# Kernel optimization log

Hardware: AMD Instinct MI355X
Metric: run time of the kernel (lower is better)

Reference implementation:

```python
import jax, jax.numpy as jnp
import numpy as np

B, NP, L, C, NA = 16, 512, 20, 3, 50
RATIO = 0.8
K = int(np.ceil(RATIO * NP))  # 410 nodes kept per graph
N = B * NP
E = 6 * N
NF, EF = 13, 4
EPS = 1e-5


def _graph_norm(x, w, b, ms):
    # PyG GraphNorm called WITHOUT batch in the source -> single global graph
    mean = x.mean(0)
    out = x - ms * mean
    var = (out * out).mean(0)
    return w * out / jnp.sqrt(var + EPS) + b


def _forward(x, pan_w, lin1_w, lin1_b, norm1_w, norm1_b, norm1_ms,
             pool_p, pool_beta, gat_wl, gat_bl, gat_wr, gat_br, gat_att, gat_bias,
             norm2_w, norm2_b, norm2_ms,
             val1_w, val1_b, val2_w, val2_b, val3_w, val3_b,
             adv1_w, adv1_b, adv2_w, adv2_b, adv3_w, adv3_b,
             edge_index, current_node_ids, action_mask):
    src, dst = edge_index[0], edge_index[1]
    # PANConv builds SparseTensor(row=edge_index[1], col=edge_index[0]) -> row = target
    A = jnp.zeros((B, NP, NP), x.dtype).at[dst // NP, dst % NP, src % NP].set(1.0)
    eyeB = jnp.broadcast_to(jnp.eye(NP, dtype=x.dtype), A.shape)

    # panentropy: M = sum_{i=0..L} w_i * A^i  (dense per graph)
    def step(carry, wi):
        tmp, acc = carry
        tmp = tmp @ A
        return (tmp, acc + wi * tmp), None
    (_, M), _ = jax.lax.scan(step, (eyeB, pan_w[0] * eyeB), pan_w[1:])
    deg = M.sum(-1)                                   # row sums
    dis = jnp.where(deg > 0, 1.0 / jnp.sqrt(deg), 0.0)
    Mn = dis[:, :, None] * M * dis[:, None, :]        # D^-1/2 M D^-1/2

    # conv1: propagate (Mn @ x) then Linear
    x3 = x.reshape(B, NP, NF)
    h = jnp.einsum('bij,bjf->bif', Mn, x3) @ lin1_w + lin1_b   # [B,NP,C]
    x1 = jax.nn.relu(_graph_norm(h.reshape(N, C), norm1_w, norm1_b, norm1_ms))  # [N,C]
    h = x1.reshape(B, NP, C)

    # PANPooling: score = tanh(b0 * <x,p> + b1 * colsum(Mn)); keep top K per graph
    score = jnp.tanh(pool_beta[0] * (h * pool_p).sum(-1) + pool_beta[1] * Mn.sum(-2))
    vals, idx = jax.lax.top_k(score, K)                        # [B,K]
    xp = jnp.take_along_axis(h, idx[:, :, None], axis=1) * vals[..., None]
    Mg = jax.vmap(lambda m, i: m[i][:, i])(Mn, idx)            # filtered adjacency [B,K,K]
    mask = (jnp.swapaxes(Mg, 1, 2) != 0) | jnp.eye(K, dtype=bool)  # mask[b,i,j]: edge j->i (+self loops)

    # GATv2Conv, heads=1, eval mode (no dropout), edge_attr not passed in source
    xl = xp @ gat_wl + gat_bl
    xr = xp @ gat_wr + gat_br
    e = jax.nn.leaky_relu(xr[:, :, None, :] + xl[:, None, :, :], 0.2)  # [B,i,j,C]
    logits = jnp.where(mask, jnp.einsum('bijc,c->bij', e, gat_att), -1e9)
    alpha = jax.nn.softmax(logits, axis=-1)
    g = jnp.einsum('bij,bjc->bic', alpha, xl) + gat_bias

    g = jax.nn.relu(_graph_norm(g.reshape(B * K, C), norm2_w, norm2_b, norm2_ms)).reshape(B, K, C)
    gp = g.sum(1)                                              # global_add_pool [B,C]

    # source uses POOLED bincount cumsum offsets to index the pre-pool arrays (faithful)
    gidx = current_node_ids + jnp.arange(B, dtype=current_node_ids.dtype) * K
    feat = jnp.concatenate([x[gidx], x1[gidx], gp], axis=1)    # [B,19]

    a = jax.nn.relu(feat @ adv1_w + adv1_b)
    a = jax.nn.relu(a @ adv2_w + adv2_b)
    a = a @ adv3_w + adv3_b
    v = jax.nn.relu(feat @ val1_w + val1_b)
    v = jax.nn.relu(v @ val2_w + val2_b)
    v = v @ val3_w + val3_b
    q = v + (a - a.mean(1, keepdims=True))
    return jnp.where(action_mask == 0, -1e8, q)


def setup_inputs() -> dict:
    key = jax.random.key(0)
    ks = list(jax.random.split(key, 40))
    nk = lambda: ks.pop()
    # within-graph random edges so the PyG-style batch structure is valid
    g = jax.random.randint(nk(), (E,), 0, B)
    u = jax.random.randint(nk(), (E,), 0, NP)
    v = jax.random.randint(nk(), (E,), 0, NP)
    edge_index = jnp.stack([g * NP + u, g * NP + v]).astype(jnp.int32)

    def lin(k, i, o):
        k1, k2 = jax.random.split(k)
        return (jax.random.normal(k1, (i, o), jnp.float32) / np.sqrt(i),
                jax.random.normal(k2, (o,), jnp.float32) * 0.01)

    lin1_w, lin1_b = lin(nk(), NF, C)
    gat_wl, gat_bl = lin(nk(), C, C)
    gat_wr, gat_br = lin(nk(), C, C)
    val1_w, val1_b = lin(nk(), 19, 10)
    val2_w, val2_b = lin(nk(), 10, 5)
    val3_w, val3_b = lin(nk(), 5, 1)
    adv1_w, adv1_b = lin(nk(), 19, 10)
    adv2_w, adv2_b = lin(nk(), 10, 5)
    adv3_w, adv3_b = lin(nk(), 5, NA)
    return dict(
        x=jax.random.normal(nk(), (N, NF), jnp.float32),
        edge_index=edge_index,
        edge_attr=jax.random.normal(nk(), (E, EF), jnp.float32),
        batch=jnp.arange(N, dtype=jnp.int32) // NP,
        current_node_ids=jax.random.randint(nk(), (B,), 0, NP),
        action_mask=jax.random.randint(nk(), (B, NA), 0, 2),
        pan_w=jax.random.uniform(nk(), (L + 1,), jnp.float32) * 0.5,
        lin1_w=lin1_w, lin1_b=lin1_b,
        norm1_w=jnp.ones(C), norm1_b=jnp.zeros(C), norm1_ms=jnp.ones(C),
        pool_p=jax.random.normal(nk(), (C,), jnp.float32),
        pool_beta=jnp.array([0.5, 0.5], jnp.float32),
        gat_wl=gat_wl, gat_bl=gat_bl, gat_wr=gat_wr, gat_br=gat_br,
        gat_att=jax.random.normal(nk(), (C,), jnp.float32),
        gat_bias=jax.random.normal(nk(), (C,), jnp.float32) * 0.01,
        norm2_w=jnp.ones(C), norm2_b=jnp.zeros(C), norm2_ms=jnp.ones(C),
        val1_w=val1_w, val1_b=val1_b, val2_w=val2_w, val2_b=val2_b,
        val3_w=val3_w, val3_b=val3_b,
        adv1_w=adv1_w, adv1_b=adv1_b, adv2_w=adv2_w, adv2_b=adv2_b,
        adv3_w=adv3_w, adv3_b=adv3_b,
    )


def reference(x, edge_index, edge_attr, batch, current_node_ids, action_mask,
              pan_w, lin1_w, lin1_b, norm1_w, norm1_b, norm1_ms,
              pool_p, pool_beta, gat_wl, gat_bl, gat_wr, gat_br, gat_att, gat_bias,
              norm2_w, norm2_b, norm2_ms,
              val1_w, val1_b, val2_w, val2_b, val3_w, val3_b,
              adv1_w, adv1_b, adv2_w, adv2_b, adv3_w, adv3_b):
    del edge_attr, batch  # received by the torch forward but never consumed
    return _forward(x, pan_w, lin1_w, lin1_b, norm1_w, norm1_b, norm1_ms,
                    pool_p, pool_beta, gat_wl, gat_bl, gat_wr, gat_br, gat_att, gat_bias,
                    norm2_w, norm2_b, norm2_ms,
                    val1_w, val1_b, val2_w, val2_b, val3_w, val3_b,
                    adv1_w, adv1_b, adv2_w, adv2_b, adv3_w, adv3_b,
                    edge_index, current_node_ids, action_mask)
```

## Files before the change

kernel.cpp:

```cpp
#include <hip/hip_runtime.h>
#include <hip/hip_bf16.h>
#include <stdint.h>
#include <math.h>

#define BB   16
#define NPn  512
#define LLp  20
#define NAa  50
#define KKk  410
#define NNt  (BB * NPn)
#define EEe  (6 * NNt)
#define NFf  13
#define KPAD 416
#define EPSf 1e-5f
#define QCLMP 1e6f
#define MAXD 28
#define PADR 512

__device__ __forceinline__ float r12_sane(float v) {
    if (!(v == v)) return 0.0f;
    return fminf(fmaxf(v, -1e15f), 1e15f);
}

__global__ __launch_bounds__(256) void r12_scatter(
    const int* __restrict__ ei,
    uint32_t* __restrict__ fwdb, uint32_t* __restrict__ trsb)
{
    const int e = blockIdx.x * 256 + threadIdx.x;
    if (e < EEe) {
        const int src = ei[e], dst = ei[EEe + e];
        atomicOr(&fwdb[(size_t)dst * 16 + ((src & 511) >> 5)], 1u << (src & 31));
        atomicOr(&trsb[(size_t)src * 16 + ((dst & 511) >> 5)], 1u << (dst & 31));
    }
}

__global__ __launch_bounds__(256) void r12_extract(
    const uint32_t* __restrict__ fwdb, const uint32_t* __restrict__ trsb,
    unsigned short* __restrict__ csrF, unsigned short* __restrict__ csrT)
{
    const int t = blockIdx.x * 256 + threadIdx.x;
    const int node = t & 8191;
    const uint32_t* bs = (t < 8192) ? (fwdb + (size_t)node * 16)
                                    : (trsb + (size_t)node * 16);
    unsigned short* cs = (t < 8192) ? csrF : csrT;
    int cnt = 0;
    for (int w = 0; w < 16; ++w) {
        uint32_t bits = bs[w];
        while (bits) {
            const int u = (w << 5) + __ffs(bits) - 1;
            bits &= bits - 1;
            if (cnt < MAXD) cs[(size_t)cnt * 8192 + node] = (unsigned short)u;
            ++cnt;
        }
    }
    for (int j = cnt; j < MAXD; ++j) cs[(size_t)j * 8192 + node] = PADR;
}

__global__ __launch_bounds__(512) void r12_deg(
    const unsigned short* __restrict__ csrF,
    const float* __restrict__ panw,
    float* __restrict__ disv)
{
    __shared__ float pa[513], pb[513];
    __shared__ float wsh[21];
    const int b = blockIdx.x, v = threadIdx.x;
    const int node = b * 512 + v;
    int iF[MAXD];
#pragma unroll
    for (int j = 0; j < MAXD; ++j) iF[j] = (int)csrF[(size_t)j * 8192 + node];
    if (v < 21) wsh[v] = panw[v];
    pa[v] = 1.0f;
    if (v == 0) { pa[512] = 0.0f; pb[512] = 0.0f; }
    __syncthreads();
    float dacc = wsh[0];
    float* rp = pa; float* rn = pb;
    for (int i = 1; i <= LLp; ++i) {
        float t[MAXD];
#pragma unroll
        for (int j = 0; j < MAXD; ++j) t[j] = rp[iF[j]];
        float s = 0.0f;
#pragma unroll
        for (int j = 0; j < MAXD; ++j) s += t[j];
        rn[v] = s;
        dacc += wsh[i] * s;
        __syncthreads();
        float* tp = rp; rp = rn; rn = tp;
    }
    disv[node] = (dacc > 0.0f) ? 1.0f / sqrtf(dacc) : 0.0f;
}

__global__ __launch_bounds__(512) void r12_chan(
    const float* __restrict__ x,
    const unsigned short* __restrict__ csrF,
    const unsigned short* __restrict__ csrT,
    const float* __restrict__ disv,
    const float* __restrict__ panw,
    const float* __restrict__ l1w,
    const float* __restrict__ l1b,
    float* __restrict__ h_raw,
    float* __restrict__ colsum)
{
    __shared__ float pa[513], pb[513];
    __shared__ float wsh[21];
    const int b = blockIdx.x, c = blockIdx.y, v = threadIdx.x;
    const int node = b * 512 + v;
    const unsigned short* csr = (c < 3) ? csrF : csrT;
    int idx[MAXD];
#pragma unroll
    for (int j = 0; j < MAXD; ++j) idx[j] = (int)csr[(size_t)j * 8192 + node];
    if (v < 21) wsh[v] = panw[v];
    const float d0 = disv[node];

    float seed;
    if (c < 3) {
        float xw = 0.0f;
        const float* xr = x + (size_t)node * NFf;
        for (int f = 0; f < NFf; ++f) xw += xr[f] * l1w[f * 3 + c];
        seed = d0 * xw;
    } else {
        seed = d0;
    }
    pa[v] = seed;
    if (v == 0) { pa[512] = 0.0f; pb[512] = 0.0f; }
    __syncthreads();
    float acc = wsh[0] * seed;
    float* rp = pa; float* rn = pb;
    for (int i = 1; i <= LLp; ++i) {
        float t[MAXD];
#pragma unroll
        for (int j = 0; j < MAXD; ++j) t[j] = rp[idx[j]];
        float s = 0.0f;
#pragma unroll
        for (int j = 0; j < MAXD; ++j) s += t[j];
        rn[v] = s;
        acc += wsh[i] * s;
        __syncthreads();
        float* tp = rp; rp = rn; rn = tp;
    }
    if (c < 3) h_raw[(size_t)node * 3 + c] = r12_sane(d0 * acc + l1b[c]);
    else       colsum[node] = r12_sane(d0 * acc);
}

__global__ __launch_bounds__(512) void r12_closure(
    const unsigned short* __restrict__ csrF, uint32_t* __restrict__ Rb)
{
    __shared__ uint32_t R1[513], R2[513];
    const int b = blockIdx.x, q = blockIdx.y, v = threadIdx.x;
    const int node = b * 512 + v;
    int iF[MAXD];
#pragma unroll
    for (int j = 0; j < MAXD; ++j) iF[j] = (int)csrF[(size_t)j * 8192 + node];
    R1[v] = ((v >> 5) == q) ? (1u << (v & 31)) : 0u;
    if (v == 0) { R1[512] = 0u; R2[512] = 0u; }
    __syncthreads();
    uint32_t* Rp = R1; uint32_t* Rn = R2;
    for (int i = 0; i < LLp; ++i) {
        uint32_t t[MAXD];
#pragma unroll
        for (int j = 0; j < MAXD; ++j) t[j] = Rp[iF[j]];
        uint32_t r = Rp[v];
#pragma unroll
        for (int j = 0; j < MAXD; ++j) r |= t[j];
        Rn[v] = r;
        __syncthreads();
        uint32_t* tp = Rp; Rp = Rn; Rn = tp;
    }
    Rb[(size_t)node * 16 + q] = Rp[v];
}

__global__ __launch_bounds__(512) void r12_pool(
    const float* __restrict__ h_raw,
    const float* __restrict__ colsum,
    const float* n1w, const float* n1b, const float* n1ms,
    const float* poolp, const float* poolb,
    float* __restrict__ x1,
    float* __restrict__ xp,
    int* __restrict__ kept)
{
    __shared__ float red[512];
    __shared__ float mv[6];
    __shared__ float sc[NPn];
    const int b = blockIdx.x, v = threadIdx.x;
    const float inv_n = 1.0f / (float)NNt;

    float hv0[16], hv1[16], hv2[16];
    float s0 = 0.0f, s1 = 0.0f, s2 = 0.0f;
#pragma unroll
    for (int k = 0; k < 16; ++k) {
        const float* hr = h_raw + (size_t)(k * 512 + v) * 3;
        hv0[k] = hr[0]; hv1[k] = hr[1]; hv2[k] = hr[2];
        s0 += hv0[k]; s1 += hv1[k]; s2 += hv2[k];
    }
    float acc[3] = { s0, s1, s2 };
    for (int c = 0; c < 3; ++c) {
        __syncthreads();
        red[v] = acc[c];
        __syncthreads();
        for (int st = 256; st > 0; st >>= 1) {
            if (v < st) red[v] += red[v + st];
            __syncthreads();
        }
        if (v == 0) mv[c] = red[0] * inv_n;
    }
    __syncthreads();
    const float mm0 = n1ms[0] * mv[0], mm1 = n1ms[1] * mv[1], mm2 = n1ms[2] * mv[2];
    float a0 = 0.0f, a1 = 0.0f, a2 = 0.0f;
#pragma unroll
    for (int k = 0; k < 16; ++k) {
        const float d0 = hv0[k] - mm0, d1 = hv1[k] - mm1, d2 = hv2[k] - mm2;
        a0 += d0 * d0; a1 += d1 * d1; a2 += d2 * d2;
    }
    float accv[3] = { a0, a1, a2 };
    for (int c = 0; c < 3; ++c) {
        __syncthreads();
        red[v] = accv[c];
        __syncthreads();
        for (int st = 256; st > 0; st >>= 1) {
            if (v < st) red[v] += red[v + st];
            __syncthreads();
        }
        if (v == 0) mv[3 + c] = red[0] * inv_n;
    }
    __syncthreads();

    const float mmv[3] = { mm0, mm1, mm2 };
    float xv[3];
#pragma unroll
    for (int c = 0; c < 3; ++c) {
        const float iv = 1.0f / sqrtf(fmaxf(mv[3 + c], 0.0f) + EPSf);
        const float o  = h_raw[(size_t)(b * NPn + v) * 3 + c] - mmv[c];
        const float tt = n1w[c] * o * iv + n1b[c];
        xv[c] = fmaxf(tt, 0.0f);
        x1[(size_t)(b * NPn + v) * 3 + c] = xv[c];
    }
    float s = poolb[0] * (xv[0] * poolp[0] + xv[1] * poolp[1] + xv[2] * poolp[2])
            + poolb[1] * colsum[b * NPn + v];
    s = tanhf(s);
    if (!(s == s)) s = 0.0f;
    sc[v] = s;
    __syncthreads();
    int cnt = 0;
    for (int u = 0; u < NPn; ++u) {
        const float su = sc[u];
        cnt += ((su > s) || (su == s && u < v)) ? 1 : 0;
    }
    if (cnt < KKk) {
        kept[b * KPAD + cnt] = v;
        xp[(size_t)(b * KPAD + cnt) * 3 + 0] = xv[0] * s;
        xp[(size_t)(b * KPAD + cnt) * 3 + 1] = xv[1] * s;
        xp[(size_t)(b * KPAD + cnt) * 3 + 2] = xv[2] * s;
    }
}

__global__ __launch_bounds__(512) void r12_gat(
    const float* __restrict__ xp,
    const int* __restrict__ kept,
    const uint32_t* __restrict__ Rb,
    const float* wl, const float* bl,
    const float* wr, const float* br,
    const float* att, const float* gbias,
    float* __restrict__ g_raw)
{
    __shared__ float xlS[KKk * 3];
    __shared__ int kidx[KPAD];
    __shared__ uint32_t RT[16 * KPAD];
    const int b = blockIdx.x, t = threadIdx.x;
    const int lane = t & 63, wv = t >> 6;
    const int wid = blockIdx.y * 8 + wv;

    float Wl[9], Wr[9];
#pragma unroll
    for (int i2 = 0; i2 < 9; ++i2) { Wl[i2] = wl[i2]; Wr[i2] = wr[i2]; }
    const float Bl0 = bl[0], Bl1 = bl[1], Bl2 = bl[2];
    const float Br0 = br[0], Br1 = br[1], Br2 = br[2];
    const float At0 = att[0], At1 = att[1], At2 = att[2];
    const float Gb0 = gbias[0], Gb1 = gbias[1], Gb2 = gbias[2];

    for (int j = t; j < KKk; j += 512) {
        const int vj = kept[b * KPAD + j];
        kidx[j] = vj;
        const float p0 = xp[(size_t)(b * KPAD + j) * 3 + 0];
        const float p1 = xp[(size_t)(b * KPAD + j) * 3 + 1];
        const float p2 = xp[(size_t)(b * KPAD + j) * 3 + 2];
        xlS[j * 3 + 0] = p0 * Wl[0] + p1 * Wl[3] + p2 * Wl[6] + Bl0;
        xlS[j * 3 + 1] = p0 * Wl[1] + p1 * Wl[4] + p2 * Wl[7] + Bl1;
        xlS[j * 3 + 2] = p0 * Wl[2] + p1 * Wl[5] + p2 * Wl[8] + Bl2;
        const uint32_t* rr = Rb + (size_t)(b * NPn + vj) * 16;
#pragma unroll
        for (int w = 0; w < 16; ++w) RT[w * KPAD + j] = rr[w];
    }
    __syncthreads();

    for (int i = wid; i < KKk; i += 32) {
        const float p0 = xp[(size_t)(b * KPAD + i) * 3 + 0];
        const float p1 = xp[(size_t)(b * KPAD + i) * 3 + 1];
        const float p2 = xp[(size_t)(b * KPAD + i) * 3 + 2];
        const float xr0 = p0 * Wr[0] + p1 * Wr[3] + p2 * Wr[6] + Br0;
        const float xr1 = p0 * Wr[1] + p1 * Wr[4] + p2 * Wr[7] + Br1;
        const float xr2 = p0 * Wr[2] + p1 * Wr[5] + p2 * Wr[8] + Br2;
        const int bi = kidx[i];
        const uint32_t mbit = 1u << (bi & 31);
        const uint32_t* Rw = &RT[(bi >> 5) * KPAD];

        float mx = -3e38f, lsum = 0.0f, a0 = 0.0f, a1 = 0.0f, a2 = 0.0f;
        for (int j = lane; j < KKk; j += 64) {
            if ((Rw[j] & mbit) || (j == i)) {
                float e0 = xr0 + xlS[j * 3 + 0]; e0 = e0 > 0.0f ? e0 : 0.2f * e0;
                float e1 = xr1 + xlS[j * 3 + 1]; e1 = e1 > 0.0f ? e1 : 0.2f * e1;
                float e2 = xr2 + xlS[j * 3 + 2]; e2 = e2 > 0.0f ? e2 : 0.2f * e2;
                const float s = At0 * e0 + At1 * e1 + At2 * e2;
                if (s > mx) {
                    const float r = __expf(mx - s);
                    lsum *= r; a0 *= r; a1 *= r; a2 *= r;
                    mx = s;
                }
                const float pj = __expf(s - mx);
                lsum += pj;
                a0 += pj * xlS[j * 3 + 0];
                a1 += pj * xlS[j * 3 + 1];
                a2 += pj * xlS[j * 3 + 2];
            }
        }
        for (int off = 32; off; off >>= 1) {
            const float mo = __shfl_xor(mx, off);
            const float lo = __shfl_xor(lsum, off);
            const float b0 = __shfl_xor(a0, off);
            const float b1 = __shfl_xor(a1, off);
            const float b2 = __shfl_xor(a2, off);
            const float M  = fmaxf(mx, mo);
            const float ea = __expf(mx - M), eb = __expf(mo - M);
            lsum = lsum * ea + lo * eb;
            a0 = a0 * ea + b0 * eb;
            a1 = a1 * ea + b1 * eb;
            a2 = a2 * ea + b2 * eb;
            mx = M;
        }
        if (lane == 0) {
            const float rl = 1.0f / fmaxf(lsum, 1e-30f);
            g_raw[(size_t)(b * KPAD + i) * 3 + 0] = r12_sane(a0 * rl + Gb0);
            g_raw[(size_t)(b * KPAD + i) * 3 + 1] = r12_sane(a1 * rl + Gb1);
            g_raw[(size_t)(b * KPAD + i) * 3 + 2] = r12_sane(a2 * rl + Gb2);
        }
    }
}

__global__ __launch_bounds__(512) void r12_head(
    const float* __restrict__ g_raw,
    const float* __restrict__ x1,
    const float* __restrict__ x,
    const int* __restrict__ cnid,
    const int* __restrict__ amask,
    const float* n2w, const float* n2b, const float* n2ms,
    const float* v1w, const float* v1b,
    const float* v2w, const float* v2b,
    const float* v3w, const float* v3b,
    const float* a1w, const float* a1b,
    const float* a2w, const float* a2b,
    const float* a3w, const float* a3b,
    float* __restrict__ out)
{
    __shared__ float rbuf[512];
    __shared__ float mv[6];
    __shared__ float gp[3];
    __shared__ float feat[19];
    __shared__ float h1a[10], h1v[10], h2a[5], h2v[5];
    __shared__ float a3[50];
    __shared__ float vout_s, amean_s;
    const int b = blockIdx.x, t = threadIdx.x;
    const float denom = 1.0f / (float)(BB * KKk);

    float gv0[13], gv1[13], gv2[13];
    float s0 = 0.0f, s1 = 0.0f, s2 = 0.0f;
#pragma unroll
    for (int k = 0; k < 13; ++k) {
        const int r = k * 512 + t;
        float q0 = 0.0f, q1 = 0.0f, q2 = 0.0f;
        if (r < BB * KKk) {
            const int bq = r / KKk, iq = r - bq * KKk;
            const float* gr = g_raw + (size_t)(bq * KPAD + iq) * 3;
            q0 = gr[0]; q1 = gr[1]; q2 = gr[2];
        }
        gv0[k] = q0; gv1[k] = q1; gv2[k] = q2;
        s0 += q0; s1 += q1; s2 += q2;
    }
    float acc[3] = { s0, s1, s2 };
    for (int c = 0; c < 3; ++c) {
        __syncthreads();
        rbuf[t] = acc[c];
        __syncthreads();
        for (int st = 256; st > 0; st >>= 1) {
            if (t < st) rbuf[t] += rbuf[t + st];
            __syncthreads();
        }
        if (t == 0) mv[c] = rbuf[0] * denom;
    }
    __syncthreads();
    const float mm0 = n2ms[0] * mv[0], mm1 = n2ms[1] * mv[1], mm2 = n2ms[2] * mv[2];
    float a0 = 0.0f, a1 = 0.0f, a2 = 0.0f;
#pragma unroll
    for (int k = 0; k < 13; ++k) {
        const int r = k * 512 + t;
        if (r < BB * KKk) {
            const float d0 = gv0[k] - mm0, d1 = gv1[k] - mm1, d2 = gv2[k] - mm2;
            a0 += d0 * d0; a1 += d1 * d1; a2 += d2 * d2;
        }
    }
    float accv[3] = { a0, a1, a2 };
    for (int c = 0; c < 3; ++c) {
        __syncthreads();
        rbuf[t] = accv[c];
        __syncthreads();
        for (int st = 256; st > 0; st >>= 1) {
            if (t < st) rbuf[t] += rbuf[t + st];
            __syncthreads();
        }
        if (t == 0) mv[3 + c] = rbuf[0] * denom;
    }
    __syncthreads();

    const float mmv[3] = { mm0, mm1, mm2 };
    float s3[3] = { 0.0f, 0.0f, 0.0f };
    if (t < KKk) {
        const size_t r = (size_t)(b * KPAD + t) * 3;
#pragma unroll
        for (int c = 0; c < 3; ++c) {
            const float iv = 1.0f / sqrtf(fmaxf(mv[3 + c], 0.0f) + EPSf);
            s3[c] = fmaxf((g_raw[r + c] - mmv[c]) * iv * n2w[c] + n2b[c], 0.0f);
        }
    }
    for (int c = 0; c < 3; ++c) {
        __syncthreads();
        rbuf[t] = s3[c];
        __syncthreads();
        for (int st = 256; st > 0; st >>= 1) {
            if (t < st) rbuf[t] += rbuf[t + st];
            __syncthreads();
        }
        if (t == 0) gp[c] = rbuf[0];
    }
    __syncthreads();

    if (t < 19) {
        const int gidx = cnid[b] + b * KKk;
        float fv;
        if (t < 13)      fv = x[(size_t)gidx * NFf + t];
        else if (t < 16) fv = x1[(size_t)gidx * 3 + (t - 13)];
        else             fv = gp[t - 16];
        feat[t] = fv;
    }
    __syncthreads();

    if (t < 10) {
        float s = a1b[t];
        for (int f = 0; f < 19; ++f) s += feat[f] * a1w[f * 10 + t];
        h1a[t] = fmaxf(s, 0.0f);
    } else if (t >= 64 && t < 74) {
        const int j = t - 64;
        float s = v1b[j];
        for (int f = 0; f < 19; ++f) s += feat[f] * v1w[f * 10 + j];
        h1v[j] = fmaxf(s, 0.0f);
    }
    __syncthreads();
    if (t < 5) {
        float s = a2b[t];
        for (int k = 0; k < 10; ++k) s += h1a[k] * a2w[k * 5 + t];
        h2a[t] = fmaxf(s, 0.0f);
    } else if (t >= 64 && t < 69) {
        const int j = t - 64;
        float s = v2b[j];
        for (int k = 0; k < 10; ++k) s += h1v[k] * v2w[k * 5 + j];
        h2v[j] = fmaxf(s, 0.0f);
    }
    __syncthreads();
    if (t < 50) {
        float s = a3b[t];
        for (int k = 0; k < 5; ++k) s += h2a[k] * a3w[k * 50 + t];
        a3[t] = s;
    } else if (t == 64) {
        float s = v3b[0];
        for (int k = 0; k < 5; ++k) s += h2v[k] * v3w[k];
        vout_s = s;
    }
    __syncthreads();
    if (t == 0) {
        float s = 0.0f;
        for (int k = 0; k < 50; ++k) s += a3[k];
        amean_s = s * (1.0f / 50.0f);
    }
    __syncthreads();
    if (t < 50) {
        float q = vout_s + a3[t] - amean_s;
        if (!(q == q)) q = 0.0f;
        q = fminf(fmaxf(q, -QCLMP), QCLMP);
        out[b * NAa + t] = (amask[b * NAa + t] == 0) ? -1e8f : q;
    }
}

extern "C" void kernel_launch(void* const* d_in, const int* in_sizes, int n_in,
                              void* d_out, int out_size, void* d_ws, size_t ws_size,
                              hipStream_t stream) {
    (void)in_sizes; (void)n_in; (void)out_size;
    const float* x     = (const float*)d_in[0];
    const int* ei      = (const int*)d_in[1];
    const int* cnid    = (const int*)d_in[4];
    const int* amask   = (const int*)d_in[5];
    const float* panw  = (const float*)d_in[6];
    const float* l1w   = (const float*)d_in[7];
    const float* l1b   = (const float*)d_in[8];
    const float* n1w   = (const float*)d_in[9];
    const float* n1b   = (const float*)d_in[10];
    const float* n1ms  = (const float*)d_in[11];
    const float* poolp = (const float*)d_in[12];
    const float* poolb = (const float*)d_in[13];
    const float* gwl   = (const float*)d_in[14];
    const float* gbl   = (const float*)d_in[15];
    const float* gwr   = (const float*)d_in[16];
    const float* gbr   = (const float*)d_in[17];
    const float* gatt  = (const float*)d_in[18];
    const float* gbias = (const float*)d_in[19];
    const float* n2w   = (const float*)d_in[20];
    const float* n2b   = (const float*)d_in[21];
    const float* n2ms  = (const float*)d_in[22];
    const float* v1w   = (const float*)d_in[23];
    const float* v1b   = (const float*)d_in[24];
    const float* v2w   = (const float*)d_in[25];
    const float* v2b   = (const float*)d_in[26];
    const float* v3w   = (const float*)d_in[27];
    const float* v3b   = (const float*)d_in[28];
    const float* a1w   = (const float*)d_in[29];
    const float* a1b   = (const float*)d_in[30];
    const float* a2w   = (const float*)d_in[31];
    const float* a2b   = (const float*)d_in[32];
    const float* a3w   = (const float*)d_in[33];
    const float* a3b   = (const float*)d_in[34];
    float* out         = (float*)d_out;

    uint8_t* wsb = (uint8_t*)d_ws;
    uint32_t* fwdb = (uint32_t*)wsb;
    uint32_t* trsb = (uint32_t*)(wsb + 524288);
    uint32_t* Rb   = trsb;
    unsigned short* csrF = (unsigned short*)(wsb + 1048576);
    unsigned short* csrT = csrF + (size_t)MAXD * 8192;
    float* h_raw  = (float*)(csrT + (size_t)MAXD * 8192);
    float* x1     = h_raw + (size_t)NNt * 3;
    float* colsum = x1 + (size_t)NNt * 3;
    float* disv   = colsum + NNt;
    float* xp     = disv + NNt;
    float* g_raw  = xp + (size_t)BB * KPAD * 3;
    int*   kept   = (int*)(g_raw + (size_t)BB * KPAD * 3);
    const size_t needed = 1048576 + 2 * (size_t)MAXD * 8192 * 2 +
                          ((size_t)(2 * NNt * 3 + 2 * NNt + 2 * BB * KPAD * 3 + BB * KPAD)) * 4;
    if (ws_size < needed) return;

    hipMemsetAsync(fwdb, 0, 1048576, stream);
    r12_scatter<<<dim3((EEe + 255) / 256), dim3(256), 0, stream>>>(ei, fwdb, trsb);
    r12_extract<<<dim3(64), dim3(256), 0, stream>>>(fwdb, trsb, csrF, csrT);
    r12_deg<<<dim3(16), dim3(512), 0, stream>>>(csrF, panw, disv);
    r12_chan<<<dim3(16, 4), dim3(512), 0, stream>>>(x, csrF, csrT, disv, panw,
                                                    l1w, l1b, h_raw, colsum);
    r12_closure<<<dim3(16, 16), dim3(512), 0, stream>>>(csrF, Rb);
    r12_pool<<<dim3(16), dim3(512), 0, stream>>>(h_raw, colsum, n1w, n1b, n1ms,
                                                 poolp, poolb, x1, xp, kept);
    r12_gat<<<dim3(16, 4), dim3(512), 0, stream>>>(xp, kept, Rb, gwl, gbl, gwr, gbr,
                                                   gatt, gbias, g_raw);
    r12_head<<<dim3(16), dim3(512), 0, stream>>>(g_raw, x1, x, cnid, amask,
                                                 n2w, n2b, n2ms, v1w, v1b, v2w, v2b, v3w, v3b,
                                                 a1w, a1b, a2w, a2b, a3w, a3b, out);
}
```

Measured before the change: 247.4 us.

## Fuse all pipeline stages into one persistent kernel with grid barriers

Replaces the eight separate kernel launches (scatter, extract, degree, channel propagation, closure, pool, GAT, head) with a single 256-block kernel. The stages are separated by a software grid barrier built from an atomic counter and a spin-wait. The aim is to remove per-launch overhead and the inter-kernel gaps in a pipeline made of many tiny kernels. In exchange it depends on all 256 blocks being resident at once, otherwise the spin barrier deadlocks. It also leaves most blocks idle in the stages that use only 16 or 64 blocks.

```diff
diff --git a/kernel.cpp b/kernel.cpp
--- a/kernel.cpp
+++ b/kernel.cpp
@@ -16,340 +16,36 @@
 #define QCLMP 1e6f
 #define MAXD 28
 #define PADR 512
-
-__device__ __forceinline__ float r12_sane(float v) {
+#define NBLK 256
+
+__device__ __forceinline__ float r13_sane(float v) {
     if (!(v == v)) return 0.0f;
     return fminf(fmaxf(v, -1e15f), 1e15f);
 }
 
-__global__ __launch_bounds__(256) void r12_scatter(
+__device__ __forceinline__ void r13_bar(uint32_t* cnt, uint32_t gen) {
+    __threadfence();
+    __syncthreads();
+    if (threadIdx.x == 0) {
+        atomicAdd(cnt, 1u);
+        while (atomicAdd(cnt, 0u) < gen * NBLK) { __builtin_amdgcn_s_sleep(8); }
+    }
+    __syncthreads();
+    __threadfence();
+}
+
+__global__ __launch_bounds__(512) void r13_mega(
+    const float* __restrict__ x,
     const int* __restrict__ ei,
-    uint32_t* __restrict__ fwdb, uint32_t* __restrict__ trsb)
-{
-    const int e = blockIdx.x * 256 + threadIdx.x;
-    if (e < EEe) {
-        const int src = ei[e], dst = ei[EEe + e];
-        atomicOr(&fwdb[(size_t)dst * 16 + ((src & 511) >> 5)], 1u << (src & 31));
-        atomicOr(&trsb[(size_t)src * 16 + ((dst & 511) >> 5)], 1u << (dst & 31));
-    }
-}
-
-__global__ __launch_bounds__(256) void r12_extract(
-    const uint32_t* __restrict__ fwdb, const uint32_t* __restrict__ trsb,
-    unsigned short* __restrict__ csrF, unsigned short* __restrict__ csrT)
-{
-    const int t = blockIdx.x * 256 + threadIdx.x;
-    const int node = t & 8191;
-    const uint32_t* bs = (t < 8192) ? (fwdb + (size_t)node * 16)
-                                    : (trsb + (size_t)node * 16);
-    unsigned short* cs = (t < 8192) ? csrF : csrT;
-    int cnt = 0;
-    for (int w = 0; w < 16; ++w) {
-        uint32_t bits = bs[w];
-        while (bits) {
-            const int u = (w << 5) + __ffs(bits) - 1;
-            bits &= bits - 1;
-            if (cnt < MAXD) cs[(size_t)cnt * 8192 + node] = (unsigned short)u;
-            ++cnt;
-        }
-    }
-    for (int j = cnt; j < MAXD; ++j) cs[(size_t)j * 8192 + node] = PADR;
-}
-
-__global__ __launch_bounds__(512) void r12_deg(
-    const unsigned short* __restrict__ csrF,
+    const int* __restrict__ cnid,
+    const int* __restrict__ amask,
     const float* __restrict__ panw,
-    float* __restrict__ disv)
-{
-    __shared__ float pa[513], pb[513];
-    __shared__ float wsh[21];
-    const int b = blockIdx.x, v = threadIdx.x;
-    const int node = b * 512 + v;
-    int iF[MAXD];
-#pragma unroll
-    for (int j = 0; j < MAXD; ++j) iF[j] = (int)csrF[(size_t)j * 8192 + node];
-    if (v < 21) wsh[v] = panw[v];
-    pa[v] = 1.0f;
-    if (v == 0) { pa[512] = 0.0f; pb[512] = 0.0f; }
-    __syncthreads();
-    float dacc = wsh[0];
-    float* rp = pa; float* rn = pb;
-    for (int i = 1; i <= LLp; ++i) {
-        float t[MAXD];
-#pragma unroll
-        for (int j = 0; j < MAXD; ++j) t[j] = rp[iF[j]];
-        float s = 0.0f;
-#pragma unroll
-        for (int j = 0; j < MAXD; ++j) s += t[j];
-        rn[v] = s;
-        dacc += wsh[i] * s;
-        __syncthreads();
-        float* tp = rp; rp = rn; rn = tp;
-    }
-    disv[node] = (dacc > 0.0f) ? 1.0f / sqrtf(dacc) : 0.0f;
-}
-
-__global__ __launch_bounds__(512) void r12_chan(
-    const float* __restrict__ x,
-    const unsigned short* __restrict__ csrF,
-    const unsigned short* __restrict__ csrT,
-    const float* __restrict__ disv,
-    const float* __restrict__ panw,
-    const float* __restrict__ l1w,
-    const float* __restrict__ l1b,
-    float* __restrict__ h_raw,
-    float* __restrict__ colsum)
-{
-    __shared__ float pa[513], pb[513];
-    __shared__ float wsh[21];
-    const int b = blockIdx.x, c = blockIdx.y, v = threadIdx.x;
-    const int node = b * 512 + v;
-    const unsigned short* csr = (c < 3) ? csrF : csrT;
-    int idx[MAXD];
-#pragma unroll
-    for (int j = 0; j < MAXD; ++j) idx[j] = (int)csr[(size_t)j * 8192 + node];
-    if (v < 21) wsh[v] = panw[v];
-    const float d0 = disv[node];
-
-    float seed;
-    if (c < 3) {
-        float xw = 0.0f;
-        const float* xr = x + (size_t)node * NFf;
-        for (int f = 0; f < NFf; ++f) xw += xr[f] * l1w[f * 3 + c];
-        seed = d0 * xw;
-    } else {
-        seed = d0;
-    }
-    pa[v] = seed;
-    if (v == 0) { pa[512] = 0.0f; pb[512] = 0.0f; }
-    __syncthreads();
-    float acc = wsh[0] * seed;
-    float* rp = pa; float* rn = pb;
-    for (int i = 1; i <= LLp; ++i) {
-        float t[MAXD];
-#pragma unroll
-        for (int j = 0; j < MAXD; ++j) t[j] = rp[idx[j]];
-        float s = 0.0f;
-#pragma unroll
-        for (int j = 0; j < MAXD; ++j) s += t[j];
-        rn[v] = s;
-        acc += wsh[i] * s;
-        __syncthreads();
-        float* tp = rp; rp = rn; rn = tp;
-    }
-    if (c < 3) h_raw[(size_t)node * 3 + c] = r12_sane(d0 * acc + l1b[c]);
-    else       colsum[node] = r12_sane(d0 * acc);
-}
-
-__global__ __launch_bounds__(512) void r12_closure(
-    const unsigned short* __restrict__ csrF, uint32_t* __restrict__ Rb)
-{
-    __shared__ uint32_t R1[513], R2[513];
-    const int b = blockIdx.x, q = blockIdx.y, v = threadIdx.x;
-    const int node = b * 512 + v;
-    int iF[MAXD];
-#pragma unroll
-    for (int j = 0; j < MAXD; ++j) iF[j] = (int)csrF[(size_t)j * 8192 + node];
-    R1[v] = ((v >> 5) == q) ? (1u << (v & 31)) : 0u;
-    if (v == 0) { R1[512] = 0u; R2[512] = 0u; }
-    __syncthreads();
-    uint32_t* Rp = R1; uint32_t* Rn = R2;
-    for (int i = 0; i < LLp; ++i) {
-        uint32_t t[MAXD];
-#pragma unroll
-        for (int j = 0; j < MAXD; ++j) t[j] = Rp[iF[j]];
-        uint32_t r = Rp[v];
-#pragma unroll
-        for (int j = 0; j < MAXD; ++j) r |= t[j];
-        Rn[v] = r;
-        __syncthreads();
-        uint32_t* tp = Rp; Rp = Rn; Rn = tp;
-    }
-    Rb[(size_t)node * 16 + q] = Rp[v];
-}
-
-__global__ __launch_bounds__(512) void r12_pool(
-    const float* __restrict__ h_raw,
-    const float* __restrict__ colsum,
+    const float* __restrict__ l1w, const float* __restrict__ l1b,
     const float* n1w, const float* n1b, const float* n1ms,
     const float* poolp, const float* poolb,
-    float* __restrict__ x1,
-    float* __restrict__ xp,
-    int* __restrict__ kept)
-{
-    __shared__ float red[512];
-    __shared__ float mv[6];
-    __shared__ float sc[NPn];
-    const int b = blockIdx.x, v = threadIdx.x;
-    const float inv_n = 1.0f / (float)NNt;
-
-    float hv0[16], hv1[16], hv2[16];
-    float s0 = 0.0f, s1 = 0.0f, s2 = 0.0f;
-#pragma unroll
-    for (int k = 0; k < 16; ++k) {
-        const float* hr = h_raw + (size_t)(k * 512 + v) * 3;
-        hv0[k] = hr[0]; hv1[k] = hr[1]; hv2[k] = hr[2];
-        s0 += hv0[k]; s1 += hv1[k]; s2 += hv2[k];
-    }
-    float acc[3] = { s0, s1, s2 };
-    for (int c = 0; c < 3; ++c) {
-        __syncthreads();
-        red[v] = acc[c];
-        __syncthreads();
-        for (int st = 256; st > 0; st >>= 1) {
-            if (v < st) red[v] += red[v + st];
-            __syncthreads();
-        }
-        if (v == 0) mv[c] = red[0] * inv_n;
-    }
-    __syncthreads();
-    const float mm0 = n1ms[0] * mv[0], mm1 = n1ms[1] * mv[1], mm2 = n1ms[2] * mv[2];
-    float a0 = 0.0f, a1 = 0.0f, a2 = 0.0f;
-#pragma unroll
-    for (int k = 0; k < 16; ++k) {
-        const float d0 = hv0[k] - mm0, d1 = hv1[k] - mm1, d2 = hv2[k] - mm2;
-        a0 += d0 * d0; a1 += d1 * d1; a2 += d2 * d2;
-    }
-    float accv[3] = { a0, a1, a2 };
-    for (int c = 0; c < 3; ++c) {
-        __syncthreads();
-        red[v] = accv[c];
-        __syncthreads();
-        for (int st = 256; st > 0; st >>= 1) {
-            if (v < st) red[v] += red[v + st];
-            __syncthreads();
-        }
-        if (v == 0) mv[3 + c] = red[0] * inv_n;
-    }
-    __syncthreads();
-
-    const float mmv[3] = { mm0, mm1, mm2 };
-    float xv[3];
-#pragma unroll
-    for (int c = 0; c < 3; ++c) {
-        const float iv = 1.0f / sqrtf(fmaxf(mv[3 + c], 0.0f) + EPSf);
-        const float o  = h_raw[(size_t)(b * NPn + v) * 3 + c] - mmv[c];
-        const float tt = n1w[c] * o * iv + n1b[c];
-        xv[c] = fmaxf(tt, 0.0f);
-        x1[(size_t)(b * NPn + v) * 3 + c] = xv[c];
-    }
-    float s = poolb[0] * (xv[0] * poolp[0] + xv[1] * poolp[1] + xv[2] * poolp[2])
-            + poolb[1] * colsum[b * NPn + v];
-    s = tanhf(s);
-    if (!(s == s)) s = 0.0f;
-    sc[v] = s;
-    __syncthreads();
-    int cnt = 0;
-    for (int u = 0; u < NPn; ++u) {
-        const float su = sc[u];
-        cnt += ((su > s) || (su == s && u < v)) ? 1 : 0;
-    }
-    if (cnt < KKk) {
-        kept[b * KPAD + cnt] = v;
-        xp[(size_t)(b * KPAD + cnt) * 3 + 0] = xv[0] * s;
-        xp[(size_t)(b * KPAD + cnt) * 3 + 1] = xv[1] * s;
-        xp[(size_t)(b * KPAD + cnt) * 3 + 2] = xv[2] * s;
-    }
-}
-
-__global__ __launch_bounds__(512) void r12_gat(
-    const float* __restrict__ xp,
-    const int* __restrict__ kept,
-    const uint32_t* __restrict__ Rb,
-    const float* wl, const float* bl,
-    const float* wr, const float* br,
-    const float* att, const float* gbias,
-    float* __restrict__ g_raw)
-{
-    __shared__ float xlS[KKk * 3];
-    __shared__ int kidx[KPAD];
-    __shared__ uint32_t RT[16 * KPAD];
-    const int b = blockIdx.x, t = threadIdx.x;
-    const int lane = t & 63, wv = t >> 6;
-    const int wid = blockIdx.y * 8 + wv;
-
-    float Wl[9], Wr[9];
-#pragma unroll
-    for (int i2 = 0; i2 < 9; ++i2) { Wl[i2] = wl[i2]; Wr[i2] = wr[i2]; }
-    const float Bl0 = bl[0], Bl1 = bl[1], Bl2 = bl[2];
-    const float Br0 = br[0], Br1 = br[1], Br2 = br[2];
-    const float At0 = att[0], At1 = att[1], At2 = att[2];
-    const float Gb0 = gbias[0], Gb1 = gbias[1], Gb2 = gbias[2];
-
-    for (int j = t; j < KKk; j += 512) {
-        const int vj = kept[b * KPAD + j];
-        kidx[j] = vj;
-        const float p0 = xp[(size_t)(b * KPAD + j) * 3 + 0];
-        const float p1 = xp[(size_t)(b * KPAD + j) * 3 + 1];
-        const float p2 = xp[(size_t)(b * KPAD + j) * 3 + 2];
-        xlS[j * 3 + 0] = p0 * Wl[0] + p1 * Wl[3] + p2 * Wl[6] + Bl0;
-        xlS[j * 3 + 1] = p0 * Wl[1] + p1 * Wl[4] + p2 * Wl[7] + Bl1;
-        xlS[j * 3 + 2] = p0 * Wl[2] + p1 * Wl[5] + p2 * Wl[8] + Bl2;
-        const uint32_t* rr = Rb + (size_t)(b * NPn + vj) * 16;
-#pragma unroll
-        for (int w = 0; w < 16; ++w) RT[w * KPAD + j] = rr[w];
-    }
-    __syncthreads();
-
-    for (int i = wid; i < KKk; i += 32) {
-        const float p0 = xp[(size_t)(b * KPAD + i) * 3 + 0];
-        const float p1 = xp[(size_t)(b * KPAD + i) * 3 + 1];
-        const float p2 = xp[(size_t)(b * KPAD + i) * 3 + 2];
-        const float xr0 = p0 * Wr[0] + p1 * Wr[3] + p2 * Wr[6] + Br0;
-        const float xr1 = p0 * Wr[1] + p1 * Wr[4] + p2 * Wr[7] + Br1;
-        const float xr2 = p0 * Wr[2] + p1 * Wr[5] + p2 * Wr[8] + Br2;
-        const int bi = kidx[i];
-        const uint32_t mbit = 1u << (bi & 31);
-        const uint32_t* Rw = &RT[(bi >> 5) * KPAD];
-
-        float mx = -3e38f, lsum = 0.0f, a0 = 0.0f, a1 = 0.0f, a2 = 0.0f;
-        for (int j = lane; j < KKk; j += 64) {
-            if ((Rw[j] & mbit) || (j == i)) {
-                float e0 = xr0 + xlS[j * 3 + 0]; e0 = e0 > 0.0f ? e0 : 0.2f * e0;
-                float e1 = xr1 + xlS[j * 3 + 1]; e1 = e1 > 0.0f ? e1 : 0.2f * e1;
-                float e2 = xr2 + xlS[j * 3 + 2]; e2 = e2 > 0.0f ? e2 : 0.2f * e2;
-                const float s = At0 * e0 + At1 * e1 + At2 * e2;
-                if (s > mx) {
-                    const float r = __expf(mx - s);
-                    lsum *= r; a0 *= r; a1 *= r; a2 *= r;
-                    mx = s;
-                }
-                const float pj = __expf(s - mx);
-                lsum += pj;
-                a0 += pj * xlS[j * 3 + 0];
-                a1 += pj * xlS[j * 3 + 1];
-                a2 += pj * xlS[j * 3 + 2];
-            }
-        }
-        for (int off = 32; off; off >>= 1) {
-            const float mo = __shfl_xor(mx, off);
-            const float lo = __shfl_xor(lsum, off);
-            const float b0 = __shfl_xor(a0, off);
-            const float b1 = __shfl_xor(a1, off);
-            const float b2 = __shfl_xor(a2, off);
-            const float M  = fmaxf(mx, mo);
-            const float ea = __expf(mx - M), eb = __expf(mo - M);
-            lsum = lsum * ea + lo * eb;
-            a0 = a0 * ea + b0 * eb;
-            a1 = a1 * ea + b1 * eb;
-            a2 = a2 * ea + b2 * eb;
-            mx = M;
-        }
-        if (lane == 0) {
-            const float rl = 1.0f / fmaxf(lsum, 1e-30f);
-            g_raw[(size_t)(b * KPAD + i) * 3 + 0] = r12_sane(a0 * rl + Gb0);
-            g_raw[(size_t)(b * KPAD + i) * 3 + 1] = r12_sane(a1 * rl + Gb1);
-            g_raw[(size_t)(b * KPAD + i) * 3 + 2] = r12_sane(a2 * rl + Gb2);
-        }
-    }
-}
-
-__global__ __launch_bounds__(512) void r12_head(
-    const float* __restrict__ g_raw,
-    const float* __restrict__ x1,
-    const float* __restrict__ x,
-    const int* __restrict__ cnid,
-    const int* __restrict__ amask,
+    const float* gwl, const float* gbl,
+    const float* gwr, const float* gbr,
+    const float* gatt, const float* gbias,
     const float* n2w, const float* n2b, const float* n2ms,
     const float* v1w, const float* v1b,
     const float* v2w, const float* v2b,
@@ -357,142 +53,437 @@
     const float* a1w, const float* a1b,
     const float* a2w, const float* a2b,
     const float* a3w, const float* a3b,
+    uint32_t* __restrict__ fwdb, uint32_t* __restrict__ trsb,
+    uint32_t* __restrict__ cnt,
+    unsigned short* __restrict__ csrF, unsigned short* __restrict__ csrT,
+    float* __restrict__ h_raw, float* __restrict__ x1,
+    float* __restrict__ colsum, float* __restrict__ disv,
+    float* __restrict__ xp, float* __restrict__ g_raw,
+    int* __restrict__ kept,
     float* __restrict__ out)
 {
-    __shared__ float rbuf[512];
-    __shared__ float mv[6];
-    __shared__ float gp[3];
-    __shared__ float feat[19];
-    __shared__ float h1a[10], h1v[10], h2a[5], h2v[5];
-    __shared__ float a3[50];
-    __shared__ float vout_s, amean_s;
-    const int b = blockIdx.x, t = threadIdx.x;
-    const float denom = 1.0f / (float)(BB * KKk);
-
-    float gv0[13], gv1[13], gv2[13];
-    float s0 = 0.0f, s1 = 0.0f, s2 = 0.0f;
-#pragma unroll
-    for (int k = 0; k < 13; ++k) {
-        const int r = k * 512 + t;
-        float q0 = 0.0f, q1 = 0.0f, q2 = 0.0f;
-        if (r < BB * KKk) {
-            const int bq = r / KKk, iq = r - bq * KKk;
-            const float* gr = g_raw + (size_t)(bq * KPAD + iq) * 3;
-            q0 = gr[0]; q1 = gr[1]; q2 = gr[2];
-        }
-        gv0[k] = q0; gv1[k] = q1; gv2[k] = q2;
-        s0 += q0; s1 += q1; s2 += q2;
-    }
-    float acc[3] = { s0, s1, s2 };
-    for (int c = 0; c < 3; ++c) {
-        __syncthreads();
-        rbuf[t] = acc[c];
-        __syncthreads();
-        for (int st = 256; st > 0; st >>= 1) {
-            if (t < st) rbuf[t] += rbuf[t + st];
-            __syncthreads();
-        }
-        if (t == 0) mv[c] = rbuf[0] * denom;
-    }
-    __syncthreads();
-    const float mm0 = n2ms[0] * mv[0], mm1 = n2ms[1] * mv[1], mm2 = n2ms[2] * mv[2];
-    float a0 = 0.0f, a1 = 0.0f, a2 = 0.0f;
-#pragma unroll
-    for (int k = 0; k < 13; ++k) {
-        const int r = k * 512 + t;
-        if (r < BB * KKk) {
-            const float d0 = gv0[k] - mm0, d1 = gv1[k] - mm1, d2 = gv2[k] - mm2;
+    __shared__ __align__(16) float smf[8704];
+    const int B = blockIdx.x, t = threadIdx.x;
+    const int gtid = B * 512 + t;
+    uint32_t* Rb = trsb;
+
+    if (gtid < EEe) {
+        const int src = ei[gtid], dst = ei[EEe + gtid];
+        atomicOr(&fwdb[(size_t)dst * 16 + ((src & 511) >> 5)], 1u << (src & 31));
+        atomicOr(&trsb[(size_t)src * 16 + ((dst & 511) >> 5)], 1u << (dst & 31));
+    }
+    r13_bar(cnt, 1);
+
+    if (gtid < 2 * NNt) {
+        const int node = gtid & 8191;
+        const uint32_t* bs = (gtid < NNt) ? (fwdb + (size_t)node * 16)
+                                          : (trsb + (size_t)node * 16);
+        unsigned short* cs = (gtid < NNt) ? csrF : csrT;
+        int c2 = 0;
+        for (int w = 0; w < 16; ++w) {
+            uint32_t bits = bs[w];
+            while (bits) {
+                const int u = (w << 5) + __ffs(bits) - 1;
+                bits &= bits - 1;
+                if (c2 < MAXD) cs[(size_t)c2 * 8192 + node] = (unsigned short)u;
+                ++c2;
+            }
+        }
+        for (int j = c2; j < MAXD; ++j) cs[(size_t)j * 8192 + node] = PADR;
+    }
+    r13_bar(cnt, 2);
+
+    if (B < BB) {
+        float* pa = smf; float* pb = smf + 513; float* wsh = smf + 1026;
+        const int node = B * 512 + t;
+        int iF[MAXD];
+#pragma unroll
+        for (int j = 0; j < MAXD; ++j) iF[j] = (int)csrF[(size_t)j * 8192 + node];
+        if (t < 21) wsh[t] = panw[t];
+        pa[t] = 1.0f;
+        if (t == 0) { pa[512] = 0.0f; pb[512] = 0.0f; }
+        __syncthreads();
+        float dacc = wsh[0];
+        float* rp = pa; float* rn = pb;
+        for (int i = 1; i <= LLp; ++i) {
+            float tv[MAXD];
+#pragma unroll
+            for (int j = 0; j < MAXD; ++j) tv[j] = rp[iF[j]];
+            float s = 0.0f;
+#pragma unroll
+            for (int j = 0; j < MAXD; ++j) s += tv[j];
+            rn[t] = s;
+            dacc += wsh[i] * s;
+            __syncthreads();
+            float* tp = rp; rp = rn; rn = tp;
+        }
+        disv[node] = (dacc > 0.0f) ? 1.0f / sqrtf(dacc) : 0.0f;
+    }
+    r13_bar(cnt, 3);
+
+    if (B < 64) {
+        float* pa = smf; float* pb = smf + 513; float* wsh = smf + 1026;
+        const int b = B >> 2, c = B & 3;
+        const int node = b * 512 + t;
+        const unsigned short* csr = (c < 3) ? csrF : csrT;
+        int idx[MAXD];
+#pragma unroll
+        for (int j = 0; j < MAXD; ++j) idx[j] = (int)csr[(size_t)j * 8192 + node];
+        if (t < 21) wsh[t] = panw[t];
+        const float d0 = disv[node];
+        float seed;
+        if (c < 3) {
+            float xw = 0.0f;
+            const float* xr = x + (size_t)node * NFf;
+            for (int f = 0; f < NFf; ++f) xw += xr[f] * l1w[f * 3 + c];
+            seed = d0 * xw;
+        } else {
+            seed = d0;
+        }
+        pa[t] = seed;
+        if (t == 0) { pa[512] = 0.0f; pb[512] = 0.0f; }
+        __syncthreads();
+        float acc = wsh[0] * seed;
+        float* rp = pa; float* rn = pb;
+        for (int i = 1; i <= LLp; ++i) {
+            float tv[MAXD];
+#pragma unroll
+            for (int j = 0; j < MAXD; ++j) tv[j] = rp[idx[j]];
+            float s = 0.0f;
+#pragma unroll
+            for (int j = 0; j < MAXD; ++j) s += tv[j];
+            rn[t] = s;
+            acc += wsh[i] * s;
+            __syncthreads();
+            float* tp = rp; rp = rn; rn = tp;
+        }
+        if (c < 3) h_raw[(size_t)node * 3 + c] = r13_sane(d0 * acc + l1b[c]);
+        else       colsum[node] = r13_sane(d0 * acc);
+        __syncthreads();
+    }
+    {
+        const int w = (B < 64) ? (192 + B) : (B - 64);
+        const int b = w >> 4, q = w & 15;
+        uint32_t* R1 = (uint32_t*)smf;
+        uint32_t* R2 = (uint32_t*)(smf + 513);
+        const int node = b * 512 + t;
+        int iF[MAXD];
+#pragma unroll
+        for (int j = 0; j < MAXD; ++j) iF[j] = (int)csrF[(size_t)j * 8192 + node];
+        R1[t] = ((t >> 5) == q) ? (1u << (t & 31)) : 0u;
+        if (t == 0) { R1[512] = 0u; R2[512] = 0u; }
+        __syncthreads();
+        uint32_t* Rp = R1; uint32_t* Rn = R2;
+        for (int i = 0; i < LLp; ++i) {
+            uint32_t tv[MAXD];
+#pragma unroll
+            for (int j = 0; j < MAXD; ++j) tv[j] = Rp[iF[j]];
+            uint32_t r = Rp[t];
+#pragma unroll
+            for (int j = 0; j < MAXD; ++j) r |= tv[j];
+            Rn[t] = r;
+            __syncthreads();
+            uint32_t* tp = Rp; Rp = Rn; Rn = tp;
+        }
+        Rb[(size_t)node * 16 + q] = Rp[t];
+    }
+    r13_bar(cnt, 4);
+
+    if (B < BB) {
+        float* red = smf; float* sc = smf + 512; float* mv = smf + 1024;
+        const int b = B, v = t;
+        const float inv_n = 1.0f / (float)NNt;
+        float hv0[16], hv1[16], hv2[16];
+        float s0 = 0.0f, s1 = 0.0f, s2 = 0.0f;
+#pragma unroll
+        for (int k = 0; k < 16; ++k) {
+            const float* hr = h_raw + (size_t)(k * 512 + v) * 3;
+            hv0[k] = hr[0]; hv1[k] = hr[1]; hv2[k] = hr[2];
+            s0 += hv0[k]; s1 += hv1[k]; s2 += hv2[k];
+        }
+        float acc[3] = { s0, s1, s2 };
+        for (int c = 0; c < 3; ++c) {
+            __syncthreads();
+            red[v] = acc[c];
+            __syncthreads();
+            for (int st = 256; st > 0; st >>= 1) {
+                if (v < st) red[v] += red[v + st];
+                __syncthreads();
+            }
+            if (v == 0) mv[c] = red[0] * inv_n;
+        }
+        __syncthreads();
+        const float mm0 = n1ms[0] * mv[0], mm1 = n1ms[1] * mv[1], mm2 = n1ms[2] * mv[2];
+        float a0 = 0.0f, a1 = 0.0f, a2 = 0.0f;
+#pragma unroll
+        for (int k = 0; k < 16; ++k) {
+            const float d0 = hv0[k] - mm0, d1 = hv1[k] - mm1, d2 = hv2[k] - mm2;
             a0 += d0 * d0; a1 += d1 * d1; a2 += d2 * d2;
         }
-    }
-    float accv[3] = { a0, a1, a2 };
-    for (int c = 0; c < 3; ++c) {
-        __syncthreads();
-        rbuf[t] = accv[c];
-        __syncthreads();
-        for (int st = 256; st > 0; st >>= 1) {
-            if (t < st) rbuf[t] += rbuf[t + st];
-            __syncthreads();
-        }
-        if (t == 0) mv[3 + c] = rbuf[0] * denom;
-    }
-    __syncthreads();
-
-    const float mmv[3] = { mm0, mm1, mm2 };
-    float s3[3] = { 0.0f, 0.0f, 0.0f };
-    if (t < KKk) {
-        const size_t r = (size_t)(b * KPAD + t) * 3;
+        float accv[3] = { a0, a1, a2 };
+        for (int c = 0; c < 3; ++c) {
+            __syncthreads();
+            red[v] = accv[c];
+            __syncthreads();
+            for (int st = 256; st > 0; st >>= 1) {
+                if (v < st) red[v] += red[v + st];
+                __syncthreads();
+            }
+            if (v == 0) mv[3 + c] = red[0] * inv_n;
+        }
+        __syncthreads();
+        const float mmv[3] = { mm0, mm1, mm2 };
+        float xv[3];
 #pragma unroll
         for (int c = 0; c < 3; ++c) {
             const float iv = 1.0f / sqrtf(fmaxf(mv[3 + c], 0.0f) + EPSf);
-            s3[c] = fmaxf((g_raw[r + c] - mmv[c]) * iv * n2w[c] + n2b[c], 0.0f);
-        }
-    }
-    for (int c = 0; c < 3; ++c) {
-        __syncthreads();
-        rbuf[t] = s3[c];
-        __syncthreads();
-        for (int st = 256; st > 0; st >>= 1) {
-            if (t < st) rbuf[t] += rbuf[t + st];
-            __syncthreads();
-        }
-        if (t == 0) gp[c] = rbuf[0];
-    }
-    __syncthreads();
-
-    if (t < 19) {
-        const int gidx = cnid[b] + b * KKk;
-        float fv;
-        if (t < 13)      fv = x[(size_t)gidx * NFf + t];
-        else if (t < 16) fv = x1[(size_t)gidx * 3 + (t - 13)];
-        else             fv = gp[t - 16];
-        feat[t] = fv;
-    }
-    __syncthreads();
-
-    if (t < 10) {
-        float s = a1b[t];
-        for (int f = 0; f < 19; ++f) s += feat[f] * a1w[f * 10 + t];
-        h1a[t] = fmaxf(s, 0.0f);
-    } else if (t >= 64 && t < 74) {
-        const int j = t - 64;
-        float s = v1b[j];
-        for (int f = 0; f < 19; ++f) s += feat[f] * v1w[f * 10 + j];
-        h1v[j] = fmaxf(s, 0.0f);
-    }
-    __syncthreads();
-    if (t < 5) {
-        float s = a2b[t];
-        for (int k = 0; k < 10; ++k) s += h1a[k] * a2w[k * 5 + t];
-        h2a[t] = fmaxf(s, 0.0f);
-    } else if (t >= 64 && t < 69) {
-        const int j = t - 64;
-        float s = v2b[j];
-        for (int k = 0; k < 10; ++k) s += h1v[k] * v2w[k * 5 + j];
-        h2v[j] = fmaxf(s, 0.0f);
-    }
-    __syncthreads();
-    if (t < 50) {
-        float s = a3b[t];
-        for (int k = 0; k < 5; ++k) s += h2a[k] * a3w[k * 50 + t];
-        a3[t] = s;
-    } else if (t == 64) {
-        float s = v3b[0];
-        for (int k = 0; k < 5; ++k) s += h2v[k] * v3w[k];
-        vout_s = s;
-    }
-    __syncthreads();
-    if (t == 0) {
-        float s = 0.0f;
-        for (int k = 0; k < 50; ++k) s += a3[k];
-        amean_s = s * (1.0f / 50.0f);
-    }
-    __syncthreads();
-    if (t < 50) {
-        float q = vout_s + a3[t] - amean_s;
-        if (!(q == q)) q = 0.0f;
-        q = fminf(fmaxf(q, -QCLMP), QCLMP);
-        out[b * NAa + t] = (amask[b * NAa + t] == 0) ? -1e8f : q;
+            const float o  = h_raw[(size_t)(b * NPn + v) * 3 + c] - mmv[c];
+            const float tt = n1w[c] * o * iv + n1b[c];
+            xv[c] = fmaxf(tt, 0.0f);
+            x1[(size_t)(b * NPn + v) * 3 + c] = xv[c];
+        }
+        float s = poolb[0] * (xv[0] * poolp[0] + xv[1] * poolp[1] + xv[2] * poolp[2])
+                + poolb[1] * colsum[b * NPn + v];
+        s = tanhf(s);
+        if (!(s == s)) s = 0.0f;
+        sc[v] = s;
+        __syncthreads();
+        int c3 = 0;
+        for (int u = 0; u < NPn; ++u) {
+            const float su = sc[u];
+            c3 += ((su > s) || (su == s && u < v)) ? 1 : 0;
+        }
+        if (c3 < KKk) {
+            kept[b * KPAD + c3] = v;
+            xp[(size_t)(b * KPAD + c3) * 3 + 0] = xv[0] * s;
+            xp[(size_t)(b * KPAD + c3) * 3 + 1] = xv[1] * s;
+            xp[(size_t)(b * KPAD + c3) * 3 + 2] = xv[2] * s;
+        }
+    }
+    r13_bar(cnt, 5);
+
+    if (B < 64) {
+        float* xlS = smf;
+        int* kidx = (int*)(smf + 1232);
+        uint32_t* RT = (uint32_t*)(smf + 1648);
+        const int b = B >> 2;
+        const int lane = t & 63, wv = t >> 6;
+        const int wid = (B & 3) * 8 + wv;
+        float Wl[9], Wr[9];
+#pragma unroll
+        for (int i2 = 0; i2 < 9; ++i2) { Wl[i2] = gwl[i2]; Wr[i2] = gwr[i2]; }
+        const float Bl0 = gbl[0], Bl1 = gbl[1], Bl2 = gbl[2];
+        const float Br0 = gbr[0], Br1 = gbr[1], Br2 = gbr[2];
+        const float At0 = gatt[0], At1 = gatt[1], At2 = gatt[2];
+        const float Gb0 = gbias[0], Gb1 = gbias[1], Gb2 = gbias[2];
+
+        for (int j = t; j < KKk; j += 512) {
+            const int vj = kept[b * KPAD + j];
+            kidx[j] = vj;
+            const float p0 = xp[(size_t)(b * KPAD + j) * 3 + 0];
+            const float p1 = xp[(size_t)(b * KPAD + j) * 3 + 1];
+            const float p2 = xp[(size_t)(b * KPAD + j) * 3 + 2];
+            xlS[j * 3 + 0] = p0 * Wl[0] + p1 * Wl[3] + p2 * Wl[6] + Bl0;
+            xlS[j * 3 + 1] = p0 * Wl[1] + p1 * Wl[4] + p2 * Wl[7] + Bl1;
+            xlS[j * 3 + 2] = p0 * Wl[2] + p1 * Wl[5] + p2 * Wl[8] + Bl2;
+            const uint32_t* rr = Rb + (size_t)(b * NPn + vj) * 16;
+#pragma unroll
+            for (int w = 0; w < 16; ++w) RT[w * KPAD + j] = rr[w];
+        }
+        __syncthreads();
+
+        for (int i = wid; i < KKk; i += 32) {
+            const float p0 = xp[(size_t)(b * KPAD + i) * 3 + 0];
+            const float p1 = xp[(size_t)(b * KPAD + i) * 3 + 1];
+            const float p2 = xp[(size_t)(b * KPAD + i) * 3 + 2];
+            const float xr0 = p0 * Wr[0] + p1 * Wr[3] + p2 * Wr[6] + Br0;
+            const float xr1 = p0 * Wr[1] + p1 * Wr[4] + p2 * Wr[7] + Br1;
+            const float xr2 = p0 * Wr[2] + p1 * Wr[5] + p2 * Wr[8] + Br2;
+            const int bi = kidx[i];
+            const uint32_t mbit = 1u << (bi & 31);
+            const uint32_t* Rw = &RT[(bi >> 5) * KPAD];
+            float mx = -3e38f, lsum = 0.0f, a0 = 0.0f, a1 = 0.0f, a2 = 0.0f;
+            for (int j = lane; j < KKk; j += 64) {
+                if ((Rw[j] & mbit) || (j == i)) {
+                    float e0 = xr0 + xlS[j * 3 + 0]; e0 = e0 > 0.0f ? e0 : 0.2f * e0;
+                    float e1 = xr1 + xlS[j * 3 + 1]; e1 = e1 > 0.0f ? e1 : 0.2f * e1;
+                    float e2 = xr2 + xlS[j * 3 + 2]; e2 = e2 > 0.0f ? e2 : 0.2f * e2;
+                    const float s = At0 * e0 + At1 * e1 + At2 * e2;
+                    if (s > mx) {
+                        const float r = __expf(mx - s);
+                        lsum *= r; a0 *= r; a1 *= r; a2 *= r;
+                        mx = s;
+                    }
+                    const float pj = __expf(s - mx);
+                    lsum += pj;
+                    a0 += pj * xlS[j * 3 + 0];
+                    a1 += pj * xlS[j * 3 + 1];
+                    a2 += pj * xlS[j * 3 + 2];
+                }
+            }
+            for (int off = 32; off; off >>= 1) {
+                const float mo = __shfl_xor(mx, off);
+                const float lo = __shfl_xor(lsum, off);
+                const float b0 = __shfl_xor(a0, off);
+                const float b1 = __shfl_xor(a1, off);
+                const float b2 = __shfl_xor(a2, off);
+                const float M  = fmaxf(mx, mo);
+                const float ea = __expf(mx - M), eb = __expf(mo - M);
+                lsum = lsum * ea + lo * eb;
+                a0 = a0 * ea + b0 * eb;
+                a1 = a1 * ea + b1 * eb;
+                a2 = a2 * ea + b2 * eb;
+                mx = M;
+            }
+            if (lane == 0) {
+                const float rl = 1.0f / fmaxf(lsum, 1e-30f);
+                g_raw[(size_t)(b * KPAD + i) * 3 + 0] = r13_sane(a0 * rl + Gb0);
+                g_raw[(size_t)(b * KPAD + i) * 3 + 1] = r13_sane(a1 * rl + Gb1);
+                g_raw[(size_t)(b * KPAD + i) * 3 + 2] = r13_sane(a2 * rl + Gb2);
+            }
+        }
+    }
+    r13_bar(cnt, 6);
+
+    if (B < BB) {
+        float* rbuf = smf;
+        float* mv   = smf + 512;
+        float* gp   = smf + 520;
+        float* feat = smf + 524;
+        float* h1a  = smf + 544;
+        float* h1v  = smf + 554;
+        float* h2a  = smf + 564;
+        float* h2v  = smf + 569;
+        float* a3   = smf + 574;
+        float* vout = smf + 624;
+        float* amean = smf + 625;
+        const int b = B;
+        const float denom = 1.0f / (float)(BB * KKk);
+
+        float gv0[13], gv1[13], gv2[13];
+        float s0 = 0.0f, s1 = 0.0f, s2 = 0.0f;
+#pragma unroll
+        for (int k = 0; k < 13; ++k) {
+            const int r = k * 512 + t;
+            float q0 = 0.0f, q1 = 0.0f, q2 = 0.0f;
+            if (r < BB * KKk) {
+                const int bq = r / KKk, iq = r - bq * KKk;
+                const float* gr = g_raw + (size_t)(bq * KPAD + iq) * 3;
+                q0 = gr[0]; q1 = gr[1]; q2 = gr[2];
+            }
+            gv0[k] = q0; gv1[k] = q1; gv2[k] = q2;
+            s0 += q0; s1 += q1; s2 += q2;
+        }
+        float acc[3] = { s0, s1, s2 };
+        for (int c = 0; c < 3; ++c) {
+            __syncthreads();
+            rbuf[t] = acc[c];
+            __syncthreads();
+            for (int st = 256; st > 0; st >>= 1) {
+                if (t < st) rbuf[t] += rbuf[t + st];
+                __syncthreads();
+            }
+            if (t == 0) mv[c] = rbuf[0] * denom;
+        }
+        __syncthreads();
+        const float mm0 = n2ms[0] * mv[0], mm1 = n2ms[1] * mv[1], mm2 = n2ms[2] * mv[2];
+        float a0 = 0.0f, a1 = 0.0f, a2 = 0.0f;
+#pragma unroll
+        for (int k = 0; k < 13; ++k) {
+            const int r = k * 512 + t;
+            if (r < BB * KKk) {
+                const float d0 = gv0[k] - mm0, d1 = gv1[k] - mm1, d2 = gv2[k] - mm2;
+                a0 += d0 * d0; a1 += d1 * d1; a2 += d2 * d2;
+            }
+        }
+        float accv[3] = { a0, a1, a2 };
+        for (int c = 0; c < 3; ++c) {
+            __syncthreads();
+            rbuf[t] = accv[c];
+            __syncthreads();
+            for (int st = 256; st > 0; st >>= 1) {
+                if (t < st) rbuf[t] += rbuf[t + st];
+                __syncthreads();
+            }
+            if (t == 0) mv[3 + c] = rbuf[0] * denom;
+        }
+        __syncthreads();
+        const float mmv[3] = { mm0, mm1, mm2 };
+        float s3[3] = { 0.0f, 0.0f, 0.0f };
+        if (t < KKk) {
+            const size_t r = (size_t)(b * KPAD + t) * 3;
+#pragma unroll
+            for (int c = 0; c < 3; ++c) {
+                const float iv = 1.0f / sqrtf(fmaxf(mv[3 + c], 0.0f) + EPSf);
+                s3[c] = fmaxf((g_raw[r + c] - mmv[c]) * iv * n2w[c] + n2b[c], 0.0f);
+            }
+        }
+        for (int c = 0; c < 3; ++c) {
+            __syncthreads();
+            rbuf[t] = s3[c];
+            __syncthreads();
+            for (int st = 256; st > 0; st >>= 1) {
+                if (t < st) rbuf[t] += rbuf[t + st];
+                __syncthreads();
+            }
+            if (t == 0) gp[c] = rbuf[0];
+        }
+        __syncthreads();
+
+        if (t < 19) {
+            const int gidx = cnid[b] + b * KKk;
+            float fv;
+            if (t < 13)      fv = x[(size_t)gidx * NFf + t];
+            else if (t < 16) fv = x1[(size_t)gidx * 3 + (t - 13)];
+            else             fv = gp[t - 16];
+            feat[t] = fv;
+        }
+        __syncthreads();
+
+        if (t < 10) {
+            float s = a1b[t];
+            for (int f = 0; f < 19; ++f) s += feat[f] * a1w[f * 10 + t];
+            h1a[t] = fmaxf(s, 0.0f);
+        } else if (t >= 64 && t < 74) {
+            const int j = t - 64;
+            float s = v1b[j];
+            for (int f = 0; f < 19; ++f) s += feat[f] * v1w[f * 10 + j];
+            h1v[j] = fmaxf(s, 0.0f);
+        }
+        __syncthreads();
+        if (t < 5) {
+            float s = a2b[t];
+            for (int k = 0; k < 10; ++k) s += h1a[k] * a2w[k * 5 + t];
+            h2a[t] = fmaxf(s, 0.0f);
+        } else if (t >= 64 && t < 69) {
+            const int j = t - 64;
+            float s = v2b[j];
+            for (int k = 0; k < 10; ++k) s += h1v[k] * v2w[k * 5 + j];
+            h2v[j] = fmaxf(s, 0.0f);
+        }
+        __syncthreads();
+        if (t < 50) {
+            float s = a3b[t];
+            for (int k = 0; k < 5; ++k) s += h2a[k] * a3w[k * 50 + t];
+            a3[t] = s;
+        } else if (t == 64) {
+            float s = v3b[0];
+            for (int k = 0; k < 5; ++k) s += h2v[k] * v3w[k];
+            *vout = s;
+        }
+        __syncthreads();
+        if (t == 0) {
+            float s = 0.0f;
+            for (int k = 0; k < 50; ++k) s += a3[k];
+            *amean = s * (1.0f / 50.0f);
+        }
+        __syncthreads();
+        if (t < 50) {
+            float q = *vout + a3[t] - *amean;
+            if (!(q == q)) q = 0.0f;
+            q = fminf(fmaxf(q, -QCLMP), QCLMP);
+            out[b * NAa + t] = (amask[b * NAa + t] == 0) ? -1e8f : q;
+        }
     }
 }
 
@@ -538,8 +529,8 @@
     uint8_t* wsb = (uint8_t*)d_ws;
     uint32_t* fwdb = (uint32_t*)wsb;
     uint32_t* trsb = (uint32_t*)(wsb + 524288);
-    uint32_t* Rb   = trsb;
-    unsigned short* csrF = (unsigned short*)(wsb + 1048576);
+    uint32_t* cnt  = (uint32_t*)(wsb + 1048576);
+    unsigned short* csrF = (unsigned short*)(wsb + 1048576 + 256);
     unsigned short* csrT = csrF + (size_t)MAXD * 8192;
     float* h_raw  = (float*)(csrT + (size_t)MAXD * 8192);
     float* x1     = h_raw + (size_t)NNt * 3;
@@ -548,22 +539,14 @@
     float* xp     = disv + NNt;
     float* g_raw  = xp + (size_t)BB * KPAD * 3;
     int*   kept   = (int*)(g_raw + (size_t)BB * KPAD * 3);
-    const size_t needed = 1048576 + 2 * (size_t)MAXD * 8192 * 2 +
+    const size_t needed = 1048576 + 256 + 2 * (size_t)MAXD * 8192 * 2 +
                           ((size_t)(2 * NNt * 3 + 2 * NNt + 2 * BB * KPAD * 3 + BB * KPAD)) * 4;
     if (ws_size < needed) return;
 
-    hipMemsetAsync(fwdb, 0, 1048576, stream);
-    r12_scatter<<<dim3((EEe + 255) / 256), dim3(256), 0, stream>>>(ei, fwdb, trsb);
-    r12_extract<<<dim3(64), dim3(256), 0, stream>>>(fwdb, trsb, csrF, csrT);
-    r12_deg<<<dim3(16), dim3(512), 0, stream>>>(csrF, panw, disv);
-    r12_chan<<<dim3(16, 4), dim3(512), 0, stream>>>(x, csrF, csrT, disv, panw,
-                                                    l1w, l1b, h_raw, colsum);
-    r12_closure<<<dim3(16, 16), dim3(512), 0, stream>>>(csrF, Rb);
-    r12_pool<<<dim3(16), dim3(512), 0, stream>>>(h_raw, colsum, n1w, n1b, n1ms,
-                                                 poolp, poolb, x1, xp, kept);
-    r12_gat<<<dim3(16, 4), dim3(512), 0, stream>>>(xp, kept, Rb, gwl, gbl, gwr, gbr,
-                                                   gatt, gbias, g_raw);
-    r12_head<<<dim3(16), dim3(512), 0, stream>>>(g_raw, x1, x, cnid, amask,
-                                                 n2w, n2b, n2ms, v1w, v1b, v2w, v2b, v3w, v3b,
-                                                 a1w, a1b, a2w, a2b, a3w, a3b, out);
+    hipMemsetAsync(fwdb, 0, 1048576 + 256, stream);
+    r13_mega<<<dim3(NBLK), dim3(512), 0, stream>>>(
+        x, ei, cnid, amask, panw, l1w, l1b, n1w, n1b, n1ms, poolp, poolb,
+        gwl, gbl, gwr, gbr, gatt, gbias, n2w, n2b, n2ms,
+        v1w, v1b, v2w, v2b, v3w, v3b, a1w, a1b, a2w, a2b, a3w, a3b,
+        fwdb, trsb, cnt, csrF, csrT, h_raw, x1, colsum, disv, xp, g_raw, kept, out);
 }
```

After: 631.0 us. 155% more time.
